# Kernel tuning notes

Hardware: AMD Instinct MI355X
Metric: run time of the kernel (lower is better)

## Reference

```python
import jax, jax.numpy as jnp
import numpy as np

HID = 96
B = 64
PF = (HID + 1) ** 3  # 912673


def setup_inputs() -> dict:
    key = jax.random.key(0)
    ks = jax.random.split(key, 6)
    s1 = 1.0 / np.sqrt(PF)
    s2 = 1.0 / np.sqrt(HID)
    s3 = 1.0 / np.sqrt(HID // 2)
    return {
        "text_x": jax.random.normal(ks[0], (B, HID), jnp.float32),
        "audio_x": jax.random.normal(ks[1], (B, HID), jnp.float32),
        "video_x": jax.random.normal(ks[2], (B, HID), jnp.float32),
        "W1": jax.random.normal(ks[3], (HID, PF), jnp.float32) * s1,
        "b1": jnp.zeros((HID,), jnp.float32),
        "W2": jax.random.normal(ks[4], (HID // 2, HID), jnp.float32) * s2,
        "b2": jnp.zeros((HID // 2,), jnp.float32),
        "W3": jax.random.normal(ks[5], (3, HID // 2), jnp.float32) * s3,
        "b3": jnp.zeros((3,), jnp.float32),
    }


def reference(text_x, audio_x, video_x, W1, b1, W2, b2, W3, b3):
    bsz = text_x.shape[0]
    ones = jnp.ones((bsz, 1), text_x.dtype)
    t = jnp.concatenate([ones, text_x], axis=1)   # [B, H+1]
    a = jnp.concatenate([ones, audio_x], axis=1)  # [B, H+1]
    v = jnp.concatenate([ones, video_x], axis=1)  # [B, H+1]
    # outer product of the three modalities, flattened: [B, (H+1)^3]
    fusion = jnp.einsum("bi,bj,bk->bijk", t, a, v).reshape(bsz, -1)
    # post-fusion MLP (dropout is identity at inference)
    h = jax.nn.relu(fusion @ W1.T + b1)
    h = jax.nn.relu(h @ W2.T + b2)
    return h @ W3.T + b3
```

## Files before the change

### kernel.cpp

```cpp
#include <hip/hip_runtime.h>
#include <stdint.h>


#define HID    96
#define NP1    97
#define ROWLEN 9409
#define BATCH  64
#define RSTR   104

typedef short bf16x8 __attribute__((ext_vector_type(8)));
typedef float f32x4  __attribute__((ext_vector_type(4)));

__device__ __forceinline__ uint32_t pack2bf(float lo, float hi) {
    union { float f; uint32_t u; } a, b; a.f = lo; b.f = hi;
    uint32_t ra = (a.u + 0x7fffu + ((a.u >> 16) & 1u)) >> 16;
    uint32_t rb = (b.u + 0x7fffu + ((b.u >> 16) & 1u)) & 0xffff0000u;
    return ra | rb;
}

__global__ __launch_bounds__(256, 3)
void fusion_gemm(const float* __restrict__ W1,
                 const float* __restrict__ text_x,
                 const float* __restrict__ audio_x,
                 const float* __restrict__ video_x,
                 float* __restrict__ h1pre)
{
    __shared__ __align__(16) short Wbf[2][NP1 * RSTR];
    __shared__ float biasF[2][NP1];

    const int tid = threadIdx.x;
    const int o   = blockIdx.x >> 3;
    const int c   = blockIdx.x & 7;
    const int ilo = (c * 97) >> 3;
    const int ihi = ((c + 1) * 97) >> 3;

    const int lane = tid & 63;
    const int wave = tid >> 6;
    const int quad = lane >> 4;
    const int col  = lane & 15;
    const int b    = wave * 16 + col;

    bf16x8 bfrag[3];
#pragma unroll
    for (int ks = 0; ks < 3; ++ks) {
        const float* vp = video_x + b * HID + ks * 32 + quad * 8;
        union { bf16x8 v; uint32_t d[4]; } u;
        u.d[0] = pack2bf(vp[0], vp[1]);
        u.d[1] = pack2bf(vp[2], vp[3]);
        u.d[2] = pack2bf(vp[4], vp[5]);
        u.d[3] = pack2bf(vp[6], vp[7]);
        bfrag[ks] = u.v;
    }

    float aval[28];
#pragma unroll
    for (int mt = 0; mt < 7; ++mt)
#pragma unroll
        for (int r = 0; r < 4; ++r) {
            int j = mt * 16 + quad * 4 + r;
            aval[mt * 4 + r] = (j == 0) ? 1.f
                             : (j <= 96 ? audio_x[b * HID + (j - 1)] : 0.f);
        }

    auto stage = [&](int ii, int pbuf) {
        const float* Wt = W1 + (long)(o * 97 + ii) * ROWLEN;
        for (int j = tid; j < NP1; j += 256) biasF[pbuf][j] = Wt[j * NP1];
        for (int w = tid; w < NP1 * 12; w += 256) {
            int j = w / 12;
            int s = w - j * 12;
            const float* p = Wt + j * NP1 + 1 + s * 8;
            uint4 q;
            q.x = pack2bf(p[0], p[1]);
            q.y = pack2bf(p[2], p[3]);
            q.z = pack2bf(p[4], p[5]);
            q.w = pack2bf(p[6], p[7]);
            *reinterpret_cast<uint4*>(&Wbf[pbuf][j * RSTR + s * 8]) = q;
        }
    };

    float sacc = 0.f;

    stage(ilo, 0);
    __syncthreads();

    for (int ii = ilo; ii < ihi; ++ii) {
        const int pb = (ii - ilo) & 1;
        if (ii + 1 < ihi) stage(ii + 1, pb ^ 1);

        f32x4 acc[7];
#pragma unroll
        for (int mt = 0; mt < 7; ++mt) acc[mt] = (f32x4){0.f, 0.f, 0.f, 0.f};
#pragma unroll
        for (int ks = 0; ks < 3; ++ks)
#pragma unroll
            for (int mt = 0; mt < 7; ++mt) {
                int j  = mt * 16 + col;
                int je = j > 96 ? 96 : j;
                bf16x8 af = *reinterpret_cast<const bf16x8*>(
                    &Wbf[pb][je * RSTR + ks * 32 + quad * 8]);
                acc[mt] = __builtin_amdgcn_mfma_f32_16x16x32_bf16(af, bfrag[ks], acc[mt], 0, 0, 0);
            }

        float s = 0.f;
#pragma unroll
        for (int mt = 0; mt < 7; ++mt)
#pragma unroll
            for (int r = 0; r < 4; ++r) {
                int j  = mt * 16 + quad * 4 + r;
                int je = j > 96 ? 96 : j;
                s += (acc[mt][r] + biasF[pb][je]) * aval[mt * 4 + r];
            }
        s += __shfl_xor(s, 16);
        s += __shfl_xor(s, 32);

        float tw = (ii == 0) ? 1.f : text_x[b * HID + (ii - 1)];
        sacc += s * tw;

        __syncthreads();
    }

    if (quad == 0) atomicAdd(&h1pre[o * BATCH + b], sacc);
}

__global__ __launch_bounds__(64)
void mlp_tail(const float* __restrict__ h1pre, const float* __restrict__ b1,
              const float* __restrict__ W2, const float* __restrict__ b2,
              const float* __restrict__ W3, const float* __restrict__ b3,
              float* __restrict__ out)
{
    __shared__ float h1s[96];
    __shared__ float h2s[48];
    const int b = blockIdx.x;
    const int t = threadIdx.x;
    for (int o = t; o < 96; o += 64) {
        float v = h1pre[o * BATCH + b] + b1[o];
        h1s[o] = v > 0.f ? v : 0.f;
    }
    __syncthreads();
    if (t < 48) {
        float acc = b2[t];
#pragma unroll 8
        for (int o = 0; o < 96; ++o) acc += W2[t * 96 + o] * h1s[o];
        h2s[t] = acc > 0.f ? acc : 0.f;
    }
    __syncthreads();
    if (t < 3) {
        float acc = b3[t];
#pragma unroll
        for (int c = 0; c < 48; ++c) acc += W3[t * 48 + c] * h2s[c];
        out[b * 3 + t] = acc;
    }
}

extern "C" void kernel_launch(void* const* d_in, const int* in_sizes, int n_in,
                              void* d_out, int out_size, void* d_ws, size_t ws_size,
                              hipStream_t stream)
{
    const float* text  = (const float*)d_in[0];
    const float* audio = (const float*)d_in[1];
    const float* video = (const float*)d_in[2];
    const float* W1    = (const float*)d_in[3];
    const float* b1    = (const float*)d_in[4];
    const float* W2    = (const float*)d_in[5];
    const float* b2    = (const float*)d_in[6];
    const float* W3    = (const float*)d_in[7];
    const float* b3    = (const float*)d_in[8];
    float* h1pre = (float*)d_ws;

    hipMemsetAsync(h1pre, 0, HID * BATCH * sizeof(float), stream);
    fusion_gemm<<<96 * 8, 256, 0, stream>>>(W1, text, audio, video, h1pre);
    mlp_tail<<<BATCH, 64, 0, stream>>>(h1pre, b1, W2, b2, W3, b3, (float*)d_out);
}
```

Baseline: 491.9 us.

## Stream W1 tiles into LDS via async global_load_lds and rebalance grid to 512 blocks

Each W1 tile (one 97x97 slab) is now fetched with contiguous 16-byte global_load_lds transfers into a raw fp32 LDS buffer, then converted to bf16 from LDS. Before, each thread issued scattered per-row global loads. The 9312 tiles are split evenly across 512 blocks, with a partial-sum atomic flush at output boundaries, and occupancy drops to 2 blocks per CU to fit the extra LDS. The intent is better streaming bandwidth over the large weight matrix and better load balance. The risks are lower occupancy and the added LDS conversion pass and barriers.

```diff
diff --git a/kernel.cpp b/kernel.cpp
--- a/kernel.cpp
+++ b/kernel.cpp
@@ -7,9 +7,14 @@
 #define ROWLEN 9409
 #define BATCH  64
 #define RSTR   104
+#define NTILE  9312
+#define WTOTAL 87616608L
+#define NCHUNK 37
 
 typedef short bf16x8 __attribute__((ext_vector_type(8)));
 typedef float f32x4  __attribute__((ext_vector_type(4)));
+typedef const float __attribute__((address_space(1)))* gfp;
+typedef float __attribute__((address_space(3)))* lfp;
 
 __device__ __forceinline__ uint32_t pack2bf(float lo, float hi) {
     union { float f; uint32_t u; } a, b; a.f = lo; b.f = hi;
@@ -18,27 +23,58 @@
     return ra | rb;
 }
 
-__global__ __launch_bounds__(256, 3)
+__global__ __launch_bounds__(256, 2)
 void fusion_gemm(const float* __restrict__ W1,
                  const float* __restrict__ text_x,
                  const float* __restrict__ audio_x,
                  const float* __restrict__ video_x,
                  float* __restrict__ h1pre)
 {
+    __shared__ __align__(16) float Wraw[NCHUNK * 256];
     __shared__ __align__(16) short Wbf[2][NP1 * RSTR];
     __shared__ float biasF[2][NP1];
 
-    const int tid = threadIdx.x;
-    const int o   = blockIdx.x >> 3;
-    const int c   = blockIdx.x & 7;
-    const int ilo = (c * 97) >> 3;
-    const int ihi = ((c + 1) * 97) >> 3;
-
+    const int tid  = threadIdx.x;
     const int lane = tid & 63;
     const int wave = tid >> 6;
     const int quad = lane >> 4;
     const int col  = lane & 15;
     const int b    = wave * 16 + col;
+
+    const int t0 = (int)(((long)blockIdx.x     * NTILE) >> 9);
+    const int t1 = (int)(((long)(blockIdx.x+1) * NTILE) >> 9);
+
+    auto dma_tile = [&](int T) {
+        const long tb = (long)T * ROWLEN - (T & 3);
+        for (int c = wave; c < NCHUNK; c += 4) {
+            long gb = tb + c * 256;
+            const float* g = W1 + gb + lane * 4;
+            float* l = &Wraw[c * 256];
+            if (gb + 256 <= WTOTAL) {
+                __builtin_amdgcn_global_load_lds((gfp)g, (lfp)l, 16, 0, 0);
+            } else {
+                f32x4 v = (f32x4){0.f, 0.f, 0.f, 0.f};
+                if (gb + lane * 4 + 4 <= WTOTAL) v = *(const f32x4*)g;
+                *(f32x4*)&Wraw[c * 256 + lane * 4] = v;
+            }
+        }
+    };
+
+    auto convert = [&](int T, int pbuf) {
+        const int sh = T & 3;
+        for (int j = tid; j < NP1; j += 256) biasF[pbuf][j] = Wraw[sh + j * NP1];
+        for (int w = tid; w < NP1 * 12; w += 256) {
+            int s = w / 97;
+            int j = w - s * 97;
+            const float* p = &Wraw[sh + j * NP1 + 1 + s * 8];
+            uint4 q;
+            q.x = pack2bf(p[0], p[1]);
+            q.y = pack2bf(p[2], p[3]);
+            q.z = pack2bf(p[4], p[5]);
+            q.w = pack2bf(p[6], p[7]);
+            *reinterpret_cast<uint4*>(&Wbf[pbuf][j * RSTR + s * 8]) = q;
+        }
+    };
 
     bf16x8 bfrag[3];
 #pragma unroll
@@ -62,30 +98,17 @@
                              : (j <= 96 ? audio_x[b * HID + (j - 1)] : 0.f);
         }
 
-    auto stage = [&](int ii, int pbuf) {
-        const float* Wt = W1 + (long)(o * 97 + ii) * ROWLEN;
-        for (int j = tid; j < NP1; j += 256) biasF[pbuf][j] = Wt[j * NP1];
-        for (int w = tid; w < NP1 * 12; w += 256) {
-            int j = w / 12;
-            int s = w - j * 12;
-            const float* p = Wt + j * NP1 + 1 + s * 8;
-            uint4 q;
-            q.x = pack2bf(p[0], p[1]);
-            q.y = pack2bf(p[2], p[3]);
-            q.z = pack2bf(p[4], p[5]);
-            q.w = pack2bf(p[6], p[7]);
-            *reinterpret_cast<uint4*>(&Wbf[pbuf][j * RSTR + s * 8]) = q;
-        }
-    };
+    dma_tile(t0);
+    __syncthreads();
+    convert(t0, 0);
 
     float sacc = 0.f;
-
-    stage(ilo, 0);
-    __syncthreads();
-
-    for (int ii = ilo; ii < ihi; ++ii) {
-        const int pb = (ii - ilo) & 1;
-        if (ii + 1 < ihi) stage(ii + 1, pb ^ 1);
+    int p = 0;
+    int ocur = t0 / 97;
+
+    for (int T = t0; T < t1; ++T) {
+        __syncthreads();
+        if (T + 1 < t1) dma_tile(T + 1);
 
         f32x4 acc[7];
 #pragma unroll
@@ -97,7 +120,7 @@
                 int j  = mt * 16 + col;
                 int je = j > 96 ? 96 : j;
                 bf16x8 af = *reinterpret_cast<const bf16x8*>(
-                    &Wbf[pb][je * RSTR + ks * 32 + quad * 8]);
+                    &Wbf[p][je * RSTR + ks * 32 + quad * 8]);
                 acc[mt] = __builtin_amdgcn_mfma_f32_16x16x32_bf16(af, bfrag[ks], acc[mt], 0, 0, 0);
             }
 
@@ -108,18 +131,28 @@
             for (int r = 0; r < 4; ++r) {
                 int j  = mt * 16 + quad * 4 + r;
                 int je = j > 96 ? 96 : j;
-                s += (acc[mt][r] + biasF[pb][je]) * aval[mt * 4 + r];
+                s += (acc[mt][r] + biasF[p][je]) * aval[mt * 4 + r];
             }
         s += __shfl_xor(s, 16);
         s += __shfl_xor(s, 32);
 
-        float tw = (ii == 0) ? 1.f : text_x[b * HID + (ii - 1)];
+        const int i = T - ocur * 97;
+        float tw = (i == 0) ? 1.f : text_x[b * HID + (i - 1)];
         sacc += s * tw;
 
-        __syncthreads();
-    }
-
-    if (quad == 0) atomicAdd(&h1pre[o * BATCH + b], sacc);
+        bool last = (T + 1 == t1);
+        if (last || (T + 1 == (ocur + 1) * 97)) {
+            if (quad == 0) atomicAdd(&h1pre[ocur * BATCH + b], sacc);
+            sacc = 0.f;
+            ocur++;
+        }
+
+        if (!last) {
+            __syncthreads();
+            convert(T + 1, p ^ 1);
+            p ^= 1;
+        }
+    }
 }
 
 __global__ __launch_bounds__(64)
@@ -168,6 +201,6 @@
     float* h1pre = (float*)d_ws;
 
     hipMemsetAsync(h1pre, 0, HID * BATCH * sizeof(float), stream);
-    fusion_gemm<<<96 * 8, 256, 0, stream>>>(W1, text, audio, video, h1pre);
+    fusion_gemm<<<512, 256, 0, stream>>>(W1, text, audio, video, h1pre);
     mlp_tail<<<BATCH, 64, 0, stream>>>(h1pre, b1, W2, b2, W3, b3, (float*)d_out);
 }
```

Result: no change. 492.6 us (+0.1%).
